# Kernel tuning notes

Hardware: AMD Instinct MI355X
Metric: run time of the kernel (lower is better)

The kernel has to match this reference:

```python
import jax, jax.numpy as jnp
import numpy as np

DECAY = 0.99          # ema_decay
BETA = 0.25           # commitment_cost
EPS = 1e-5            # Laplace smoothing epsilon (haiku VQ-EMA default)
NUM_CODES = 1024
EMA_COUNTER = 1000    # prior EMA steps, for zero-debias


def setup_inputs() -> dict:
    key = jax.random.key(0)
    ks = jax.random.split(key, 8)
    B, T, D = 32768, 3, 256
    E, H, C = 512, 512, 64  # embedding_dim, mlp hidden, code_dim

    def lin(k, i, o):
        # VarianceScaling(scale=2.0) fan_in
        return jax.random.normal(k, (i, o), jnp.float32) * (2.0 / i) ** 0.5

    return dict(
        states=jax.random.normal(ks[0], (B, T, D), jnp.float32),
        w_se=lin(ks[1], D, E), b_se=jnp.zeros((E,), jnp.float32),
        w0=lin(ks[2], E, H), b0=jnp.zeros((H,), jnp.float32),
        w1=lin(ks[3], H, H), b1=jnp.zeros((H,), jnp.float32),
        w2=lin(ks[4], H, C), b2=jnp.zeros((C,), jnp.float32),
        embeddings=jax.random.normal(ks[5], (C, NUM_CODES), jnp.float32),  # haiku layout (embedding_dim, num_embeddings)
        ema_cluster_hidden=jax.random.uniform(ks[6], (NUM_CODES,), jnp.float32) * 100.0,
        ema_dw_hidden=jax.random.normal(ks[7], (C, NUM_CODES), jnp.float32),
    )


def reference(states, w_se, b_se, w0, b0, w1, b1, w2, b2,
              embeddings, ema_cluster_hidden, ema_dw_hidden):
    gelu = jax.nn.gelu  # tanh approximation, matches flax nn.gelu default
    # state embed (hk.Linear) then gelu, then MLP policy head with activate_final=True
    x = gelu(states @ w_se + b_se)          # (B,T,E)
    x = gelu(x @ w0 + b0)                   # (B,T,H)
    x = gelu(x @ w1 + b1)                   # (B,T,H)
    latent = gelu(x @ w2 + b2)              # (B,T,C) latent actions

    # --- hk.nets.VectorQuantizerEMA forward ---
    C = embeddings.shape[0]
    flat = latent.reshape(-1, C)            # (N,C)
    distances = (jnp.sum(flat ** 2, 1, keepdims=True)
                 - 2.0 * flat @ embeddings
                 + jnp.sum(embeddings ** 2, 0, keepdims=True))  # (N,K)
    idx = jnp.argmax(-distances, 1)         # nearest code per token
    encodings = jax.nn.one_hot(idx, NUM_CODES, dtype=distances.dtype)  # (N,K)
    enc_idx = idx.reshape(latent.shape[:-1])  # (B,T)
    quantized = embeddings.T[enc_idx]       # (B,T,C) codebook gather

    e_latent_loss = jnp.mean((jax.lax.stop_gradient(quantized) - latent) ** 2)

    # EMA state updates (is_training=True), with zero-debias
    debias = 1.0 - DECAY ** (EMA_COUNTER + 1)
    cl_hidden = ema_cluster_hidden * DECAY + jnp.sum(encodings, 0) * (1.0 - DECAY)
    cluster_size = cl_hidden / debias       # (K,)
    dw = flat.T @ encodings                 # (C,K) one-hot scatter of inputs
    dw_hidden = ema_dw_hidden * DECAY + dw * (1.0 - DECAY)
    updated_ema_dw = dw_hidden / debias
    n = jnp.sum(cluster_size)
    stable_cluster_size = (cluster_size + EPS) / (n + NUM_CODES * EPS) * n
    new_embeddings = updated_ema_dw / stable_cluster_size[None, :]

    loss = BETA * e_latent_loss
    quantized = latent + jax.lax.stop_gradient(quantized - latent)  # straight-through
    avg_probs = jnp.mean(encodings, 0)
    perplexity = jnp.exp(-jnp.sum(avg_probs * jnp.log(avg_probs + 1e-10)))

    return quantized, loss, perplexity, enc_idx, new_embeddings
```

## Files before the change

### kernel.cpp

```cpp
#include <hip/hip_runtime.h>
#include <hip/hip_bf16.h>
#include <math.h>

#define NTOK 98304
#define DIN  256
#define DE   512
#define DH   512
#define DC   64
#define NCODE 1024
#define CHUNK 49152
#define DWCHUNK 1024
#define HBLK 96

typedef _Float16 half8 __attribute__((ext_vector_type(8)));
typedef float f32x4 __attribute__((ext_vector_type(4)));

__device__ __forceinline__ float gelu_f(float x) {
    const float k1 = 0.044715f;
    const float C = -(2.0f * 1.4426950408889634f * 0.7978845608028654f);
    float q = x * x;
    float r = fmaf(k1, q, 1.0f);
    float t = x * r * C;
    float e = __builtin_amdgcn_exp2f(t);
    float s = __builtin_amdgcn_rcpf(e + 1.0f);
    return x * s;
}

__device__ __forceinline__ void gload_lds16(const _Float16* g, _Float16* l) {
    __builtin_amdgcn_global_load_lds(
        (const __attribute__((address_space(1))) void*)g,
        (__attribute__((address_space(3))) void*)l, 16, 0, 0);
}

__device__ __forceinline__ void raw_barrier() {
    asm volatile("s_barrier" ::: "memory");
}
__device__ __forceinline__ void lgkm0_barrier() {
    asm volatile("s_waitcnt lgkmcnt(0)" ::: "memory");
    asm volatile("s_barrier" ::: "memory");
}

__device__ __forceinline__ void tsplit_elem(const float* __restrict__ W,
                                            _Float16* __restrict__ Bh,
                                            _Float16* __restrict__ Bl,
                                            int e, int N)
{
    int k = e / N, n = e % N;
    float v = W[e];
    _Float16 h = (_Float16)v;
    _Float16 l = (_Float16)(v - (float)h);
    size_t o = ((size_t)(k >> 3) * N + n) * 8 + (k & 7);
    Bh[o] = h; Bl[o] = l;
}

__global__ __launch_bounds__(256)
void prep_all(const float* __restrict__ w_se, const float* __restrict__ w0,
              const float* __restrict__ w1, const float* __restrict__ w2,
              _Float16* __restrict__ wseh, _Float16* __restrict__ wsel,
              _Float16* __restrict__ w0h, _Float16* __restrict__ w0l,
              _Float16* __restrict__ w1h, _Float16* __restrict__ w1l,
              _Float16* __restrict__ w2h, _Float16* __restrict__ w2l,
              const float* __restrict__ emb, _Float16* __restrict__ ebh,
              _Float16* __restrict__ ebl, float* __restrict__ embT,
              float* __restrict__ e2)
{
    const int b = blockIdx.x, tid = threadIdx.x;
    if (b < 512) {
        tsplit_elem(w_se, wseh, wsel, b * 256 + tid, DE);
    } else if (b < 1536) {
        tsplit_elem(w0, w0h, w0l, (b - 512) * 256 + tid, DH);
    } else if (b < 2560) {
        tsplit_elem(w1, w1h, w1l, (b - 1536) * 256 + tid, DH);
    } else if (b < 2688) {
        tsplit_elem(w2, w2h, w2l, (b - 2560) * 256 + tid, DC);
    } else if (b < 2944) {
        int e = (b - 2688) * 256 + tid;
        int c = e >> 10, n = e & 1023;
        float v = emb[e];
        _Float16 h = (_Float16)v;
        _Float16 l = (_Float16)(v - (float)h);
        ebh[(size_t)n * DC + c] = h;
        ebl[(size_t)n * DC + c] = l;
        embT[(size_t)n * DC + c] = v;
    } else {
        int n = (b - 2944) * 256 + tid;
        float s = 0.f;
#pragma unroll
        for (int c = 0; c < DC; ++c) { float e = emb[(size_t)c * NCODE + n]; s = fmaf(e, e, s); }
        e2[n] = s;
    }
}

template<int BN, bool A_FM, bool EMIT_FM>
__global__ __launch_bounds__(256, 2)
void gemm_fm(const void* __restrict__ A0, const void* __restrict__ A1,
             const _Float16* __restrict__ Bhp, const _Float16* __restrict__ Blp,
             const float* __restrict__ bias,
             void* __restrict__ C0, void* __restrict__ C1,
             int M, int N, int K)
{
    constexpr int BM = 128;
    constexpr int WGM = (BN == 128) ? 2 : 4;
    constexpr int WAVE_M = BM / WGM;
    constexpr int MT = WAVE_M / 16;
    constexpr int NT = 4;
    constexpr int NSHIFT = (BN == 128) ? 7 : 6;
    constexpr int BCALLS = (BN * 4) / 256;

    __shared__ __align__(16) _Float16 As[2][4][BM][8];
    __shared__ __align__(16) _Float16 Bs[2][4][BN][8];

    const int tid  = threadIdx.x;
    const int lane = tid & 63, wid = tid >> 6;
    const int lm   = lane & 15, quad = lane >> 4;
    const int wave_m = (BN == 128) ? (wid & 1) * 64 : wid * 32;
    const int wave_n = (BN == 128) ? (wid >> 1) * 64 : 0;

    int bx = blockIdx.x, by = blockIdx.y;
    if (gridDim.x == 4 && (gridDim.y & 7) == 0) {
        int L = by * 4 + bx;
        int c = L & 7, w = L >> 3;
        bx = w & 3;
        by = (w >> 2) * 8 + c;
    }
    const int m0 = by * BM, n0 = bx * BN;

    f32x4 acc[MT][NT];
#pragma unroll
    for (int mi = 0; mi < MT; ++mi)
#pragma unroll
        for (int ni = 0; ni < NT; ++ni) acc[mi][ni] = (f32x4)(0.f);

    for (int k0 = 0; k0 < K; k0 += 32) {
        const int kb0 = k0 >> 3;

        if (A_FM) {
            const _Float16* ap[2] = {(const _Float16*)A0, (const _Float16*)A1};
#pragma unroll
            for (int p = 0; p < 2; ++p)
#pragma unroll
                for (int j = 0; j < 2; ++j) {
                    int e  = j * 256 + tid;
                    int kb = e >> 7, tk = e & 127;
                    const _Float16* src = ap[p] + ((size_t)(kb0 + kb) * M + m0 + tk) * 8;
                    int eb = j * 256 + (tid & ~63);
                    gload_lds16(src, &As[p][eb >> 7][eb & 127][0]);
                }
        } else {
            const float* A = (const float*)A0;
#pragma unroll
            for (int i = 0; i < 4; ++i) {
                int s = tid + i * 256;
                int row = s >> 3, kc = (s & 7) * 4;
                int kb = kc >> 3, off = kc & 7;
                float4 v = *(const float4*)(A + (size_t)(m0 + row) * K + k0 + kc);
                float vv[4] = {v.x, v.y, v.z, v.w};
                unsigned short h[4], l[4];
#pragma unroll
                for (int j = 0; j < 4; ++j) {
                    _Float16 hh = (_Float16)vv[j];
                    _Float16 ll = (_Float16)(vv[j] - (float)hh);
                    h[j] = __builtin_bit_cast(unsigned short, hh);
                    l[j] = __builtin_bit_cast(unsigned short, ll);
                }
                uint2 ph, pl;
                ph.x = (unsigned int)h[0] | ((unsigned int)h[1] << 16);
                ph.y = (unsigned int)h[2] | ((unsigned int)h[3] << 16);
                pl.x = (unsigned int)l[0] | ((unsigned int)l[1] << 16);
                pl.y = (unsigned int)l[2] | ((unsigned int)l[3] << 16);
                *(uint2*)&As[0][kb][row][off] = ph;
                *(uint2*)&As[1][kb][row][off] = pl;
            }
        }

        {
            const _Float16* bp[2] = {Bhp, Blp};
#pragma unroll
            for (int p = 0; p < 2; ++p)
#pragma unroll
                for (int j = 0; j < BCALLS; ++j) {
                    int e  = j * 256 + tid;
                    int kb = e >> NSHIFT, n = e & (BN - 1);
                    const _Float16* src = bp[p] + ((size_t)(kb0 + kb) * N + n0 + n) * 8;
                    int eb = j * 256 + (tid & ~63);
                    gload_lds16(src, &Bs[p][eb >> NSHIFT][eb & (BN - 1)][0]);
                }
        }
        __syncthreads();

        half8 ahf[MT], alf[MT], bhf[NT], blf[NT];
#pragma unroll
        for (int mi = 0; mi < MT; ++mi) {
            int r = wave_m + mi * 16 + lm;
            ahf[mi] = *(const half8*)&As[0][quad][r][0];
            alf[mi] = *(const half8*)&As[1][quad][r][0];
        }
#pragma unroll
        for (int ni = 0; ni < NT; ++ni) {
            int c = wave_n + ni * 16 + lm;
            bhf[ni] = *(const half8*)&Bs[0][quad][c][0];
            blf[ni] = *(const half8*)&Bs[1][quad][c][0];
        }
#pragma unroll
        for (int mi = 0; mi < MT; ++mi)
#pragma unroll
            for (int ni = 0; ni < NT; ++ni) {
                acc[mi][ni] = __builtin_amdgcn_mfma_f32_16x16x32_f16(ahf[mi], bhf[ni], acc[mi][ni], 0, 0, 0);
                acc[mi][ni] = __builtin_amdgcn_mfma_f32_16x16x32_f16(ahf[mi], blf[ni], acc[mi][ni], 0, 0, 0);
                acc[mi][ni] = __builtin_amdgcn_mfma_f32_16x16x32_f16(alf[mi], bhf[ni], acc[mi][ni], 0, 0, 0);
            }
        __syncthreads();
    }

#pragma unroll
    for (int ni = 0; ni < NT; ++ni) {
        int col = n0 + wave_n + ni * 16 + lm;
        float bv = bias[col];
        size_t slab = EMIT_FM ? ((size_t)(col >> 3) * M * 8 + (col & 7)) : 0;
#pragma unroll
        for (int mi = 0; mi < MT; ++mi) {
            int rowbase = m0 + wave_m + mi * 16 + quad * 4;
#pragma unroll
            for (int r = 0; r < 4; ++r) {
                float g = gelu_f(acc[mi][ni][r] + bv);
                if (EMIT_FM) {
                    _Float16 hh = (_Float16)g;
                    _Float16 ll = (_Float16)(g - (float)hh);
                    size_t oo = slab + (size_t)(rowbase + r) * 8;
                    ((_Float16*)C0)[oo] = hh;
                    ((_Float16*)C1)[oo] = ll;
                } else {
                    ((float*)C0)[(size_t)(rowbase + r) * N + col] = g;
                }
            }
        }
    }
}

__global__ __launch_bounds__(256, 2)
void vq_dist_kernel(const float* __restrict__ lat,
                    const _Float16* __restrict__ ebh, const _Float16* __restrict__ ebl,
                    const float* __restrict__ e2, const float* __restrict__ embT,
                    float* __restrict__ encidx_out, int* __restrict__ codes_out,
                    float* __restrict__ quant_out, float* __restrict__ sum_sq)
{
    __shared__ __align__(16) char Bt[16384];
    __shared__ float e2s[NCODE];
    __shared__ int sidx[128];
    __shared__ float wred[4];

    const int tid = threadIdx.x, lane = tid & 63, wave = tid >> 6;
    const int lm = lane & 15, quad = lane >> 4;
    const int tok0 = blockIdx.x * 128;

    half8 ah[2][2], al[2][2];
#pragma unroll
    for (int mt = 0; mt < 2; ++mt)
#pragma unroll
        for (int ks = 0; ks < 2; ++ks) {
            const float* ap = lat + (size_t)(tok0 + wave * 32 + mt * 16 + lm) * DC + ks * 32 + quad * 8;
            float4 v0 = *(const float4*)ap;
            float4 v1 = *(const float4*)(ap + 4);
            float vv[8] = {v0.x, v0.y, v0.z, v0.w, v1.x, v1.y, v1.z, v1.w};
            half8 hh, ll;
#pragma unroll
            for (int j = 0; j < 8; ++j) {
                _Float16 h = (_Float16)vv[j];
                hh[j] = h;
                ll[j] = (_Float16)(vv[j] - (float)h);
            }
            ah[mt][ks] = hh;
            al[mt][ks] = ll;
        }

#pragma unroll
    for (int i = 0; i < 4; ++i) { int k = tid + i * 256; e2s[k] = e2[k]; }

    const _Float16* srcbase[4];
    int ldsoff[4];
#pragma unroll
    for (int k = 0; k < 4; ++k) {
        int S = tid + (k << 8);
        int r = (S & 511) >> 3, c16 = S & 7;
        srcbase[k] = ((S < 512) ? ebh : ebl) + (r << 6) + (c16 << 3);
        ldsoff[k] = ((S >> 9) << 13) + (r << 7) + ((c16 ^ (r & 7)) << 4);
    }

    uint4 stg[4];
#pragma unroll
    for (int k = 0; k < 4; ++k) stg[k] = *(const uint4*)(srcbase[k]);
#pragma unroll
    for (int k = 0; k < 4; ++k) *(uint4*)(Bt + ldsoff[k]) = stg[k];
#pragma unroll
    for (int k = 0; k < 4; ++k) stg[k] = *(const uint4*)(srcbase[k] + 4096);
    lgkm0_barrier();

    const char* Bhi = (const char*)Bt;
    const char* Blo = (const char*)Bt + 8192;

    f32x4 acc[2][4];
    float bd[2][4]; int bi[2][4];
#pragma unroll
    for (int mt = 0; mt < 2; ++mt)
#pragma unroll
        for (int r = 0; r < 4; ++r) { bd[mt][r] = INFINITY; bi[mt][r] = 0; }

    for (int t = 0; t < 16; ++t) {
        const int k0 = t * 64;
#pragma unroll
        for (int mt = 0; mt < 2; ++mt)
#pragma unroll
            for (int ni = 0; ni < 4; ++ni) acc[mt][ni] = (f32x4)(0.f);

#pragma unroll
        for (int ks = 0; ks < 2; ++ks) {
            half8 bh[4], bl[4];
#pragma unroll
            for (int ni = 0; ni < 4; ++ni) {
                int cl = ni * 16 + lm;
                int sw = ((ks * 4 + quad) ^ (cl & 7)) << 4;
                bh[ni] = *(const half8*)(Bhi + (cl << 7) + sw);
                bl[ni] = *(const half8*)(Blo + (cl << 7) + sw);
            }
#pragma unroll
            for (int ni = 0; ni < 4; ++ni)
#pragma unroll
                for (int mt = 0; mt < 2; ++mt) {
                    acc[mt][ni] = __builtin_amdgcn_mfma_f32_16x16x32_f16(ah[mt][ks], bh[ni], acc[mt][ni], 0, 0, 0);
                    acc[mt][ni] = __builtin_amdgcn_mfma_f32_16x16x32_f16(ah[mt][ks], bl[ni], acc[mt][ni], 0, 0, 0);
                    acc[mt][ni] = __builtin_amdgcn_mfma_f32_16x16x32_f16(al[mt][ks], bh[ni], acc[mt][ni], 0, 0, 0);
                    acc[mt][ni] = __builtin_amdgcn_mfma_f32_16x16x32_f16(al[mt][ks], bl[ni], acc[mt][ni], 0, 0, 0);
                }
        }

#pragma unroll
        for (int ni = 0; ni < 4; ++ni) {
            int code = k0 + ni * 16 + lm;
            float ee = e2s[code];
#pragma unroll
            for (int mt = 0; mt < 2; ++mt)
#pragma unroll
                for (int r = 0; r < 4; ++r) {
                    float d = ee - 2.f * acc[mt][ni][r];
                    if (d < bd[mt][r]) { bd[mt][r] = d; bi[mt][r] = code; }
                }
        }

        raw_barrier();
        if (t < 15) {
#pragma unroll
            for (int k = 0; k < 4; ++k) *(uint4*)(Bt + ldsoff[k]) = stg[k];
            if (t < 14) {
#pragma unroll
                for (int k = 0; k < 4; ++k)
                    stg[k] = *(const uint4*)(srcbase[k] + (size_t)(t + 2) * 4096);
            }
            lgkm0_barrier();
        }
    }

#pragma unroll
    for (int mt = 0; mt < 2; ++mt)
#pragma unroll
        for (int r = 0; r < 4; ++r) {
            float d = bd[mt][r]; int i0 = bi[mt][r];
#pragma unroll
            for (int off = 1; off < 16; off <<= 1) {
                float od = __shfl_xor(d, off, 64);
                int   oi = __shfl_xor(i0, off, 64);
                if (od < d || (od == d && oi < i0)) { d = od; i0 = oi; }
            }
            if (lm == 0) {
                int tok = wave * 32 + mt * 16 + quad * 4 + r;
                sidx[tok] = i0;
                encidx_out[tok0 + tok] = (float)i0;
                codes_out[tok0 + tok] = i0;
            }
        }
    __syncthreads();

    const int t2 = tid >> 1;
    const int g  = tid & 1;
    const int code = sidx[t2];
    float lsum = 0.f;
#pragma unroll
    for (int q = 0; q < 4; ++q) {
        int c0 = g * 32 + q * 8;
        const size_t tb = (size_t)(tok0 + t2) * DC + c0;
        float4 x0 = *(const float4*)(lat + tb);
        float4 x1 = *(const float4*)(lat + tb + 4);
        float4 e0 = *(const float4*)(embT + (size_t)code * DC + c0);
        float4 e1 = *(const float4*)(embT + (size_t)code * DC + c0 + 4);
        float xx[8] = {x0.x, x0.y, x0.z, x0.w, x1.x, x1.y, x1.z, x1.w};
        float qq[8] = {e0.x, e0.y, e0.z, e0.w, e1.x, e1.y, e1.z, e1.w};
#pragma unroll
        for (int j = 0; j < 8; ++j) {
            float d = qq[j] - xx[j];
            lsum = fmaf(d, d, lsum);
        }
        *(float4*)(quant_out + tb) = e0;
        *(float4*)(quant_out + tb + 4) = e1;
    }
#pragma unroll
    for (int o = 32; o > 0; o >>= 1) lsum += __shfl_down(lsum, o);
    if (lane == 0) wred[wave] = lsum;
    __syncthreads();
    if (tid == 0) atomicAdd(sum_sq, wred[0] + wred[1] + wred[2] + wred[3]);
}

__global__ __launch_bounds__(256)
void hist_rank_kernel(const int* __restrict__ codes, int* __restrict__ crank,
                      unsigned int* __restrict__ hist2d)
{
    __shared__ unsigned int hist[NCODE];
    const int tid = threadIdx.x, b = blockIdx.x;
#pragma unroll
    for (int j = 0; j < 4; ++j) hist[tid + j * 256] = 0;
    __syncthreads();
#pragma unroll
    for (int j = 0; j < 4; ++j) {
        int t = b * 1024 + j * 256 + tid;
        int c = codes[t];
        crank[t] = (int)atomicAdd(&hist[c], 1u);
    }
    __syncthreads();
#pragma unroll
    for (int j = 0; j < 4; ++j) {
        int k = tid + j * 256;
        hist2d[(size_t)b * NCODE + k] = hist[k];
    }
}

__global__ __launch_bounds__(1024)
void scan_kernel(const unsigned int* __restrict__ hist2d,
                 unsigned int* __restrict__ counts, int* __restrict__ offs,
                 int* __restrict__ base2d)
{
    __shared__ int s[1024];
    const int t = threadIdx.x;
    int v = 0;
    for (int b = 0; b < HBLK; ++b) v += (int)hist2d[(size_t)b * NCODE + t];
    counts[t] = (unsigned int)v;
    s[t] = v; __syncthreads();
    for (int d = 1; d < 1024; d <<= 1) {
        int x = (t >= d) ? s[t - d] : 0;
        __syncthreads();
        s[t] += x;
        __syncthreads();
    }
    int run = s[t] - v;
    offs[t] = run;
    for (int b = 0; b < HBLK; ++b) {
        base2d[(size_t)b * NCODE + t] = run;
        run += (int)hist2d[(size_t)b * NCODE + t];
    }
}

__global__ __launch_bounds__(256)
void scatter_kernel(const int* __restrict__ codes, const int* __restrict__ crank,
                    const int* __restrict__ base2d, int* __restrict__ bucket)
{
    const int tid = threadIdx.x, b = blockIdx.x;
#pragma unroll
    for (int j = 0; j < 4; ++j) {
        int t = b * 1024 + j * 256 + tid;
        int c = codes[t];
        bucket[base2d[(size_t)b * NCODE + c] + crank[t]] = t;
    }
}

__global__ __launch_bounds__(256)
void dw_kernel(const float* __restrict__ lat, const int* __restrict__ bucket,
               const int* __restrict__ offs, const unsigned int* __restrict__ counts,
               float* __restrict__ dw)
{
    __shared__ float sred[4][64];
    const int code = blockIdx.x;
    const int n = (int)counts[code];
    const int start = blockIdx.y * DWCHUNK;
    if (start >= n) return;
    const int cnt = min(n - start, DWCHUNK);
    const int base = offs[code] + start;
    const int lane = threadIdx.x & 63, wave = threadIdx.x >> 6;

    float s0 = 0.f, s1 = 0.f, s2 = 0.f, s3 = 0.f;
    int i = wave;
    for (; i + 12 < cnt; i += 16) {
        int t0 = bucket[base + i];
        int t1 = bucket[base + i + 4];
        int t2 = bucket[base + i + 8];
        int t3 = bucket[base + i + 12];
        s0 += lat[(size_t)t0 * DC + lane];
        s1 += lat[(size_t)t1 * DC + lane];
        s2 += lat[(size_t)t2 * DC + lane];
        s3 += lat[(size_t)t3 * DC + lane];
    }
    for (; i < cnt; i += 4)
        s0 += lat[(size_t)bucket[base + i] * DC + lane];

    sred[wave][lane] = (s0 + s1) + (s2 + s3);
    __syncthreads();
    if (threadIdx.x < 64) {
        float tot = sred[0][lane] + sred[1][lane] + sred[2][lane] + sred[3][lane];
        atomicAdd(&dw[(size_t)lane * NCODE + code], tot);
    }
}

__global__ __launch_bounds__(1024)
void finalize_scalars(const unsigned int* __restrict__ counts,
                      const float* __restrict__ ema_ch,
                      const float* __restrict__ sum_sq,
                      float* __restrict__ nbuf,
                      float* __restrict__ out_loss, float* __restrict__ out_perp)
{
    __shared__ float sred[1024];
    const int k = threadIdx.x;
    const float debias = (float)(1.0 - pow(0.99, 1001.0));
    float cnt = (float)counts[k];
    float cs  = (ema_ch[k] * 0.99f + cnt * 0.01f) / debias;

    sred[k] = cs; __syncthreads();
    for (int s = 512; s > 0; s >>= 1) { if (k < s) sred[k] += sred[k + s]; __syncthreads(); }
    float n = sred[0];
    __syncthreads();

    float p = cnt / 98304.0f;
    sred[k] = p * logf(p + 1e-10f);
    __syncthreads();
    for (int s = 512; s > 0; s >>= 1) { if (k < s) sred[k] += sred[k + s]; __syncthreads(); }
    if (k == 0) {
        nbuf[0] = n;
        out_perp[0] = expf(-sred[0]);
        out_loss[0] = 0.25f * sum_sq[0] / 6291456.0f;
    }
}

__global__ __launch_bounds__(256)
void newemb_kernel(const unsigned int* __restrict__ counts,
                   const float* __restrict__ dw,
                   const float* __restrict__ ema_ch,
                   const float* __restrict__ ema_dw,
                   const float* __restrict__ nbuf,
                   float* __restrict__ out_newemb)
{
    const int e = blockIdx.x * 256 + threadIdx.x;
    const int k = e & 1023;
    const float debias = (float)(1.0 - pow(0.99, 1001.0));
    float cs = (ema_ch[k] * 0.99f + (float)counts[k] * 0.01f) / debias;
    float n = nbuf[0];
    float stable = (cs + 1e-5f) / (n + 1024.0f * 1e-5f) * n;
    out_newemb[e] = ((ema_dw[e] * 0.99f + dw[e] * 0.01f) / debias) / stable;
}

extern "C" void kernel_launch(void* const* d_in, const int* in_sizes, int n_in,
                              void* d_out, int out_size, void* d_ws, size_t ws_size,
                              hipStream_t stream)
{
    (void)in_sizes; (void)n_in; (void)out_size; (void)ws_size;
    const float* states = (const float*)d_in[0];
    const float* w_se   = (const float*)d_in[1];
    const float* b_se   = (const float*)d_in[2];
    const float* w0     = (const float*)d_in[3];
    const float* b0     = (const float*)d_in[4];
    const float* w1     = (const float*)d_in[5];
    const float* b1     = (const float*)d_in[6];
    const float* w2     = (const float*)d_in[7];
    const float* b2     = (const float*)d_in[8];
    const float* emb    = (const float*)d_in[9];
    const float* ema_ch = (const float*)d_in[10];
    const float* ema_dw = (const float*)d_in[11];

    float* out        = (float*)d_out;
    float* q_out      = out;
    float* loss_out   = out + 6291456;
    float* perp_out   = out + 6291457;
    float* idx_out    = out + 6291458;
    float* newemb_out = out + 6389762;

    char* ws = (char*)d_ws;
    size_t o = 0;
    unsigned int* counts  = (unsigned int*)(ws + o); o += 4096;
    float*        sumsq   = (float*)(ws + o);        o += 256;
    float*        dwb     = (float*)(ws + o);        o += (size_t)DC * NCODE * 4;
    const size_t ZERO_BYTES = o;
    int*          offs    = (int*)(ws + o);          o += 4096;
    int*          codes   = (int*)(ws + o);          o += (size_t)NTOK * 4;
    int*          crank   = (int*)(ws + o);          o += (size_t)NTOK * 4;
    int*          bucket  = (int*)(ws + o);          o += (size_t)NTOK * 4;
    float*        e2b     = (float*)(ws + o);        o += 4096;
    unsigned int* hist2d  = (unsigned int*)(ws + o); o += (size_t)HBLK * NCODE * 4;
    int*          base2d  = (int*)(ws + o);          o += (size_t)HBLK * NCODE * 4;
    _Float16*     ebh     = (_Float16*)(ws + o);     o += (size_t)NCODE * DC * 2;
    _Float16*     ebl     = (_Float16*)(ws + o);     o += (size_t)NCODE * DC * 2;
    float*        embT    = (float*)(ws + o);        o += (size_t)NCODE * DC * 4;
    _Float16*     wseh    = (_Float16*)(ws + o);     o += (size_t)DIN * DE * 2;
    _Float16*     wsel    = (_Float16*)(ws + o);     o += (size_t)DIN * DE * 2;
    _Float16*     w0h     = (_Float16*)(ws + o);     o += (size_t)DE * DH * 2;
    _Float16*     w0l     = (_Float16*)(ws + o);     o += (size_t)DE * DH * 2;
    _Float16*     w1h     = (_Float16*)(ws + o);     o += (size_t)DH * DH * 2;
    _Float16*     w1l     = (_Float16*)(ws + o);     o += (size_t)DH * DH * 2;
    _Float16*     w2h     = (_Float16*)(ws + o);     o += (size_t)DH * DC * 2;
    _Float16*     w2l     = (_Float16*)(ws + o);     o += (size_t)DH * DC * 2;
    _Float16*     bufAh   = (_Float16*)(ws + o);     o += (size_t)CHUNK * DE * 2;
    _Float16*     bufAl   = (_Float16*)(ws + o);     o += (size_t)CHUNK * DE * 2;
    _Float16*     bufBh   = (_Float16*)(ws + o);     o += (size_t)CHUNK * DH * 2;
    _Float16*     bufBl   = (_Float16*)(ws + o);     o += (size_t)CHUNK * DH * 2;
    float*        lat     = (float*)(ws + o);        o += (size_t)NTOK * DC * 4;

    hipMemsetAsync(d_ws, 0, ZERO_BYTES, stream);

    prep_all<<<dim3(2948), dim3(256), 0, stream>>>(
        w_se, w0, w1, w2, wseh, wsel, w0h, w0l, w1h, w1l, w2h, w2l,
        emb, ebh, ebl, embT, e2b);

    dim3 blk(256);
    const int MBLK = CHUNK / 128;
    for (int c = 0; c < NTOK / CHUNK; ++c) {
        size_t off = (size_t)c * CHUNK;
        gemm_fm<128, false, true><<<dim3(DE / 128, MBLK), blk, 0, stream>>>(
            states + off * DIN, nullptr, wseh, wsel, b_se, bufAh, bufAl, CHUNK, DE, DIN);
        gemm_fm<128, true, true><<<dim3(DH / 128, MBLK), blk, 0, stream>>>(
            bufAh, bufAl, w0h, w0l, b0, bufBh, bufBl, CHUNK, DH, DE);
        gemm_fm<128, true, true><<<dim3(DH / 128, MBLK), blk, 0, stream>>>(
            bufBh, bufBl, w1h, w1l, b1, bufAh, bufAl, CHUNK, DH, DH);
        gemm_fm<64, true, false><<<dim3(1, MBLK), blk, 0, stream>>>(
            bufAh, bufAl, w2h, w2l, b2, lat + off * DC, nullptr, CHUNK, DC, DH);
    }

    vq_dist_kernel<<<dim3(NTOK / 128), blk, 0, stream>>>(
        lat, ebh, ebl, e2b, embT, idx_out, codes, q_out, sumsq);

    hist_rank_kernel<<<dim3(HBLK), blk, 0, stream>>>(codes, crank, hist2d);
    scan_kernel<<<dim3(1), dim3(1024), 0, stream>>>(hist2d, counts, offs, base2d);
    scatter_kernel<<<dim3(HBLK), blk, 0, stream>>>(codes, crank, base2d, bucket);
    dw_kernel<<<dim3(NCODE, NTOK / DWCHUNK), blk, 0, stream>>>(lat, bucket, offs, counts, dwb);

    finalize_scalars<<<dim3(1), dim3(1024), 0, stream>>>(counts, ema_ch, sumsq,
                                                         sumsq + 1, loss_out, perp_out);
    newemb_kernel<<<dim3(256), blk, 0, stream>>>(counts, dwb, ema_ch, ema_dw,
                                                 sumsq + 1, newemb_out);
}
```

Measured before the change: 811.2 us.

## Fuse final MLP layer GEMM with VQ distance/argmin kernel per chunk

The last linear layer (H->C with gelu) is computed inside the VQ kernel, and the latent tile is kept in shared memory. Distance, argmin and quantization then read it from LDS instead of from global memory, which removes one kernel launch and a global round trip of the latents. The latents are still written to global for the dw kernel. Shared memory per block grows to about 59KB, which may limit occupancy, and the distance stage now runs per chunk with fewer blocks.

```diff
diff --git a/kernel.cpp b/kernel.cpp
--- a/kernel.cpp
+++ b/kernel.cpp
@@ -238,29 +238,116 @@
 }
 
 __global__ __launch_bounds__(256, 2)
-void vq_dist_kernel(const float* __restrict__ lat,
-                    const _Float16* __restrict__ ebh, const _Float16* __restrict__ ebl,
-                    const float* __restrict__ e2, const float* __restrict__ embT,
-                    float* __restrict__ encidx_out, int* __restrict__ codes_out,
-                    float* __restrict__ quant_out, float* __restrict__ sum_sq)
-{
-    __shared__ __align__(16) char Bt[16384];
-    __shared__ float e2s[NCODE];
+void vq_fused_kernel(const _Float16* __restrict__ Ah, const _Float16* __restrict__ Al,
+                     const _Float16* __restrict__ w2h, const _Float16* __restrict__ w2l,
+                     const float* __restrict__ b2,
+                     const _Float16* __restrict__ ebh, const _Float16* __restrict__ ebl,
+                     const float* __restrict__ e2, const float* __restrict__ embT,
+                     float* __restrict__ lat, float* __restrict__ encidx_out,
+                     int* __restrict__ codes_out, float* __restrict__ quant_out,
+                     float* __restrict__ sum_sq, int M)
+{
+    __shared__ __align__(16) char smem[34816 + 24576];
+    float (*latile)[68] = (float(*)[68])smem;
+    auto As = (_Float16 (*)[4][128][8])(smem + 34816);
+    auto Bs = (_Float16 (*)[4][64][8])(smem + 34816 + 16384);
+    char* Bt = smem + 34816;
+    float* e2s = (float*)(smem + 34816 + 16384);
     __shared__ int sidx[128];
     __shared__ float wred[4];
 
     const int tid = threadIdx.x, lane = tid & 63, wave = tid >> 6;
     const int lm = lane & 15, quad = lane >> 4;
     const int tok0 = blockIdx.x * 128;
+    const int m0 = tok0;
+
+    {
+        const int wave_m = wave * 32;
+        f32x4 acc[2][4];
+#pragma unroll
+        for (int mi = 0; mi < 2; ++mi)
+#pragma unroll
+            for (int ni = 0; ni < 4; ++ni) acc[mi][ni] = (f32x4)(0.f);
+
+        const _Float16* ap[2] = {Ah, Al};
+        const _Float16* bp[2] = {w2h, w2l};
+        for (int k0 = 0; k0 < DH; k0 += 32) {
+            const int kb0 = k0 >> 3;
+#pragma unroll
+            for (int p = 0; p < 2; ++p)
+#pragma unroll
+                for (int j = 0; j < 2; ++j) {
+                    int e  = j * 256 + tid;
+                    int kb = e >> 7, tk = e & 127;
+                    const _Float16* src = ap[p] + ((size_t)(kb0 + kb) * M + m0 + tk) * 8;
+                    int eb = j * 256 + (tid & ~63);
+                    gload_lds16(src, &As[p][eb >> 7][eb & 127][0]);
+                }
+#pragma unroll
+            for (int p = 0; p < 2; ++p) {
+                int e  = tid;
+                int kb = e >> 6, n = e & 63;
+                const _Float16* src = bp[p] + ((size_t)(kb0 + kb) * DC + n) * 8;
+                int eb = (tid & ~63);
+                gload_lds16(src, &Bs[p][eb >> 6][eb & 63][0]);
+            }
+            __syncthreads();
+
+            half8 ahf[2], alf[2], bhf[4], blf[4];
+#pragma unroll
+            for (int mi = 0; mi < 2; ++mi) {
+                int r = wave_m + mi * 16 + lm;
+                ahf[mi] = *(const half8*)&As[0][quad][r][0];
+                alf[mi] = *(const half8*)&As[1][quad][r][0];
+            }
+#pragma unroll
+            for (int ni = 0; ni < 4; ++ni) {
+                int c = ni * 16 + lm;
+                bhf[ni] = *(const half8*)&Bs[0][quad][c][0];
+                blf[ni] = *(const half8*)&Bs[1][quad][c][0];
+            }
+#pragma unroll
+            for (int mi = 0; mi < 2; ++mi)
+#pragma unroll
+                for (int ni = 0; ni < 4; ++ni) {
+                    acc[mi][ni] = __builtin_amdgcn_mfma_f32_16x16x32_f16(ahf[mi], bhf[ni], acc[mi][ni], 0, 0, 0);
+                    acc[mi][ni] = __builtin_amdgcn_mfma_f32_16x16x32_f16(ahf[mi], blf[ni], acc[mi][ni], 0, 0, 0);
+                    acc[mi][ni] = __builtin_amdgcn_mfma_f32_16x16x32_f16(alf[mi], bhf[ni], acc[mi][ni], 0, 0, 0);
+                }
+            __syncthreads();
+        }
+
+#pragma unroll
+        for (int ni = 0; ni < 4; ++ni) {
+            int col = ni * 16 + lm;
+            float bv = b2[col];
+#pragma unroll
+            for (int mi = 0; mi < 2; ++mi) {
+                int rowbase = wave_m + mi * 16 + quad * 4;
+#pragma unroll
+                for (int r = 0; r < 4; ++r) {
+                    latile[rowbase + r][col] = gelu_f(acc[mi][ni][r] + bv);
+                }
+            }
+        }
+    }
+    __syncthreads();
+
+#pragma unroll
+    for (int i = 0; i < 8; ++i) {
+        int idx = i * 256 + tid;
+        int row = idx >> 4, c4 = (idx & 15) * 4;
+        *(float4*)(lat + (size_t)(tok0 + row) * DC + c4) = *(const float4*)&latile[row][c4];
+    }
 
     half8 ah[2][2], al[2][2];
 #pragma unroll
     for (int mt = 0; mt < 2; ++mt)
 #pragma unroll
         for (int ks = 0; ks < 2; ++ks) {
-            const float* ap = lat + (size_t)(tok0 + wave * 32 + mt * 16 + lm) * DC + ks * 32 + quad * 8;
-            float4 v0 = *(const float4*)ap;
-            float4 v1 = *(const float4*)(ap + 4);
+            const float* aprow = &latile[wave * 32 + mt * 16 + lm][ks * 32 + quad * 8];
+            float4 v0 = *(const float4*)aprow;
+            float4 v1 = *(const float4*)(aprow + 4);
             float vv[8] = {v0.x, v0.y, v0.z, v0.w, v1.x, v1.y, v1.z, v1.w};
             half8 hh, ll;
 #pragma unroll
@@ -272,6 +359,7 @@
             ah[mt][ks] = hh;
             al[mt][ks] = ll;
         }
+    __syncthreads();
 
 #pragma unroll
     for (int i = 0; i < 4; ++i) { int k = tid + i * 256; e2s[k] = e2[k]; }
@@ -387,8 +475,8 @@
     for (int q = 0; q < 4; ++q) {
         int c0 = g * 32 + q * 8;
         const size_t tb = (size_t)(tok0 + t2) * DC + c0;
-        float4 x0 = *(const float4*)(lat + tb);
-        float4 x1 = *(const float4*)(lat + tb + 4);
+        float4 x0 = *(const float4*)&latile[t2][c0];
+        float4 x1 = *(const float4*)&latile[t2][c0 + 4];
         float4 e0 = *(const float4*)(embT + (size_t)code * DC + c0);
         float4 e1 = *(const float4*)(embT + (size_t)code * DC + c0 + 4);
         float xx[8] = {x0.x, x0.y, x0.z, x0.w, x1.x, x1.y, x1.z, x1.w};
@@ -623,12 +711,11 @@
             bufAh, bufAl, w0h, w0l, b0, bufBh, bufBl, CHUNK, DH, DE);
         gemm_fm<128, true, true><<<dim3(DH / 128, MBLK), blk, 0, stream>>>(
             bufBh, bufBl, w1h, w1l, b1, bufAh, bufAl, CHUNK, DH, DH);
-        gemm_fm<64, true, false><<<dim3(1, MBLK), blk, 0, stream>>>(
-            bufAh, bufAl, w2h, w2l, b2, lat + off * DC, nullptr, CHUNK, DC, DH);
-    }
-
-    vq_dist_kernel<<<dim3(NTOK / 128), blk, 0, stream>>>(
-        lat, ebh, ebl, e2b, embT, idx_out, codes, q_out, sumsq);
+        vq_fused_kernel<<<dim3(MBLK), blk, 0, stream>>>(
+            bufAh, bufAl, w2h, w2l, b2, ebh, ebl, e2b, embT,
+            lat + off * DC, idx_out + off, codes + off, q_out + off * DC,
+            sumsq, CHUNK);
+    }
 
     hist_rank_kernel<<<dim3(HBLK), blk, 0, stream>>>(codes, crank, hist2d);
     scan_kernel<<<dim3(1), dim3(1024), 0, stream>>>(hist2d, counts, offs, base2d);
```

After: 902.1 us. +11.2%, slower.
